# Optimization experiments

Hardware: AMD Instinct MI355X
Metric: run time of the kernel (lower is better)

Reference implementation:

```python
import jax, jax.numpy as jnp
import numpy as np

EMBED = 1024
HEADS = 16
HEAD_SIZE = EMBED // HEADS


def setup_inputs() -> dict:
    key = jax.random.key(0)
    ks = jax.random.split(key, 12)
    B, S = 2, 2048
    s = 1.0 / np.sqrt(EMBED)
    return {
        "querys": jax.random.normal(ks[0], (B, S, EMBED), jnp.float32),
        "keys": jax.random.normal(ks[1], (B, S, EMBED), jnp.float32),
        "values": jax.random.normal(ks[2], (B, S, EMBED), jnp.float32),
        "Wq": jax.random.normal(ks[3], (EMBED, EMBED), jnp.float32) * s,
        "bq": jax.random.normal(ks[4], (EMBED,), jnp.float32) * s,
        "Wk": jax.random.normal(ks[5], (EMBED, EMBED), jnp.float32) * s,
        "bk": jax.random.normal(ks[6], (EMBED,), jnp.float32) * s,
        "Wv": jax.random.normal(ks[7], (EMBED, EMBED), jnp.float32) * s,
        "bv": jax.random.normal(ks[8], (EMBED,), jnp.float32) * s,
        "Wo": jax.random.normal(ks[9], (EMBED, EMBED), jnp.float32) * s,
        "bo": jax.random.normal(ks[10], (EMBED,), jnp.float32) * s,
    }


def reference(querys, keys, values, Wq, bq, Wk, bk, Wv, bv, Wo, bo):
    B, S, E = querys.shape
    H, D = HEADS, HEAD_SIZE
    # torch nn.Linear: y = x @ W.T + b
    q = (querys @ Wq.T + bq).reshape(B, S, H, D).transpose(0, 2, 1, 3)  # [B,H,S,D]
    k = (keys @ Wk.T + bk).reshape(B, S, H, D).transpose(0, 2, 1, 3)
    v = (values @ Wv.T + bv).reshape(B, S, H, D).transpose(0, 2, 1, 3)
    # NOTE: original scales by head_size**0.05 (faithful to source, likely a bug)
    scale = D ** 0.05
    energy = jnp.einsum("bhqd,bhkd->bhqk", q, k) / scale  # [B,H,S,S]
    attention = jax.nn.softmax(energy, axis=-1)
    out = jnp.einsum("bhqk,bhkd->bhqd", attention, v)  # [B,H,S,D]
    out = out.transpose(0, 2, 1, 3).reshape(B, S, E)
    return out @ Wo.T + bo
```

## Files before the change

kernel.cpp:

```cpp
#include <hip/hip_runtime.h>

typedef __attribute__((ext_vector_type(4))) float f32x4;
typedef __attribute__((ext_vector_type(8))) float f32x8;
typedef __attribute__((ext_vector_type(8))) unsigned short ushort8;
typedef __attribute__((ext_vector_type(4))) unsigned short ushort4v;
typedef __attribute__((ext_vector_type(8))) __bf16 bf16x8;

#define QSCALE 1.17183256f

#if __has_builtin(__builtin_amdgcn_exp2f)
#define EXP2(x) __builtin_amdgcn_exp2f(x)
#else
#define EXP2(x) exp2f(x)
#endif

__device__ __forceinline__ unsigned short f2bf(float x) {
  unsigned u = __float_as_uint(x);
  u += 0x7FFFu + ((u >> 16) & 1u);
  return (unsigned short)(u >> 16);
}

__device__ __forceinline__ ushort8 cvt8(const float* src) {
  float4 x0 = *(const float4*)src;
  float4 x1 = *(const float4*)(src + 4);
  ushort8 v;
  v[0] = f2bf(x0.x); v[1] = f2bf(x0.y); v[2] = f2bf(x0.z); v[3] = f2bf(x0.w);
  v[4] = f2bf(x1.x); v[5] = f2bf(x1.y); v[6] = f2bf(x1.z); v[7] = f2bf(x1.w);
  return v;
}

__device__ __forceinline__ f32x4 mfma16(ushort8 a, ushort8 b, f32x4 c) {
  return __builtin_amdgcn_mfma_f32_16x16x32_bf16(
      __builtin_bit_cast(bf16x8, a), __builtin_bit_cast(bf16x8, b), c, 0, 0, 0);
}
__device__ __forceinline__ f32x4 mfma16b(bf16x8 a, ushort8 b, f32x4 c) {
  return __builtin_amdgcn_mfma_f32_16x16x32_bf16(
      a, __builtin_bit_cast(bf16x8, b), c, 0, 0, 0);
}

__device__ __forceinline__ void gload_lds16(const void* g, void* l) {
  __builtin_amdgcn_global_load_lds(
      (const __attribute__((address_space(1))) void*)g,
      (__attribute__((address_space(3))) void*)l, 16, 0, 0);
}

__global__ __launch_bounds__(256) void cvt_f32_bf16(
    const float* __restrict__ s0, const float* __restrict__ s1, const float* __restrict__ s2,
    const float* __restrict__ s3, const float* __restrict__ s4, const float* __restrict__ s5,
    const float* __restrict__ s6, unsigned short* __restrict__ dstA,
    unsigned short* __restrict__ dstW)
{
  const int z = blockIdx.y;
  const float* src;
  unsigned short* dst;
  int n;
  if (z < 3) {
    src = (z == 0) ? s0 : (z == 1) ? s1 : s2;
    dst = dstA + (size_t)z * 4194304;
    n = 4194304;
  } else {
    src = (z == 3) ? s3 : (z == 4) ? s4 : (z == 5) ? s5 : s6;
    dst = dstW + (size_t)(z - 3) * 1048576;
    n = 1048576;
  }
  int i = (blockIdx.x * 256 + threadIdx.x) * 8;
  const int stride = gridDim.x * 256 * 8;
  for (; i < n; i += stride) *(ushort8*)(dst + i) = cvt8(src + i);
}

__global__ __launch_bounds__(256) void gemm_qkv_bf(
    const unsigned short* __restrict__ Abf, const unsigned short* __restrict__ Wbf,
    const float* __restrict__ bq, const float* __restrict__ bk, const float* __restrict__ bv,
    unsigned short* __restrict__ Qb, unsigned short* __restrict__ Kb,
    unsigned short* __restrict__ Vtb)
{
  __shared__ __align__(16) unsigned short Sl[4][4096];
  const int lin = blockIdx.x + 8 * blockIdx.y + 256 * blockIdx.z;
  const int swz = (lin & 7) * 96 + (lin >> 3);
  const int bx = swz & 7, by = (swz >> 3) & 31, z = swz >> 8;

  const unsigned short* Ap = Abf + (size_t)z * 4194304;
  const unsigned short* Wp = Wbf + (size_t)z * 1048576;
  const float* bp = (z == 0) ? bq : (z == 1) ? bk : bv;

  const int t = threadIdx.x, l = t & 63, w = t >> 6;
  const int lr = l & 15, g = l >> 4;
  const int wm = (w >> 1) * 64, wn = (w & 1) * 64;

  int prow[2], pcol[2];
#pragma unroll
  for (int j = 0; j < 2; ++j) {
    int p = j * 256 + w * 64 + l;
    prow[j] = p >> 2;
    pcol[j] = (p & 3) ^ ((prow[j] >> 1) & 3);
  }

  char* lds0 = (char*)&Sl[0][0];
  const int arow0 = wm + lr, brow0 = wn + lr;
  const int abyte = (arow0 * 32 + (g ^ ((arow0 >> 1) & 3)) * 8) * 2;
  const int bbyte = 8192 + (brow0 * 32 + (g ^ ((brow0 >> 1) & 3)) * 8) * 2;

  f32x4 acc[4][4] = {};

#define STAGE_QKV(bufoff, k0)                                                     \
  {                                                                               \
    _Pragma("unroll") for (int j = 0; j < 2; ++j) {                               \
      gload_lds16(Ap + (size_t)(by * 128 + prow[j]) * 1024 + (k0) + pcol[j] * 8,  \
                  lds0 + (bufoff) + (j * 256 + w * 64) * 16);                     \
      gload_lds16(Wp + (size_t)(bx * 128 + prow[j]) * 1024 + (k0) + pcol[j] * 8,  \
                  lds0 + (bufoff) + 8192 + (j * 256 + w * 64) * 16);              \
    }                                                                             \
  }

  STAGE_QKV(0, 0)
  __syncthreads();

  for (int kt = 0; kt < 32; ++kt) {
    const int curoff = (kt & 1) << 14;
    if (kt < 31) STAGE_QKV(curoff ^ 16384, (kt + 1) * 32)
    const char* pa = lds0 + curoff;
    ushort8 a[4], b[4];
#pragma unroll
    for (int m = 0; m < 4; ++m)
      a[m] = *(const ushort8*)(pa + abyte + m * 1024);
#pragma unroll
    for (int n = 0; n < 4; ++n)
      b[n] = *(const ushort8*)(pa + bbyte + n * 1024);
#pragma unroll
    for (int m = 0; m < 4; ++m)
#pragma unroll
      for (int n = 0; n < 4; ++n)
        acc[m][n] = mfma16(a[m], b[n], acc[m][n]);
    __syncthreads();
  }

  float bias_n[4];
#pragma unroll
  for (int n = 0; n < 4; ++n) bias_n[n] = bp[bx * 128 + wn + n * 16 + lr];

  if (z < 2) {
    const float sc = (z == 0) ? QSCALE : 1.0f;
    unsigned short* Cp = z ? Kb : Qb;
#pragma unroll
    for (int m = 0; m < 4; ++m)
#pragma unroll
      for (int n = 0; n < 4; ++n)
#pragma unroll
        for (int r = 0; r < 4; ++r) {
          float v = (acc[m][n][r] + bias_n[n]) * sc;
          int gm = by * 128 + wm + m * 16 + g * 4 + r;
          int gn = bx * 128 + wn + n * 16 + lr;
          int bb = gm >> 11, s = gm & 2047;
          int h = gn >> 6, d = gn & 63;
          Cp[((size_t)((bb * 16 + h) * 2048 + s) << 6) + d] = f2bf(v);
        }
  } else {
#pragma unroll
    for (int m = 0; m < 4; ++m) {
      int gm0 = by * 128 + wm + m * 16 + g * 4;
      int bb = gm0 >> 11, s0 = gm0 & 2047;
#pragma unroll
      for (int n = 0; n < 4; ++n) {
        int gn = bx * 128 + wn + n * 16 + lr;
        int h = gn >> 6, d = gn & 63;
        ushort4v pk;
#pragma unroll
        for (int r = 0; r < 4; ++r) pk[r] = f2bf(acc[m][n][r] + bias_n[n]);
        *(ushort4v*)&Vtb[((size_t)((bb * 16 + h) * 64 + d) << 11) + s0] = pk;
      }
    }
  }
}

__global__ __launch_bounds__(256) void gemm_o_bf(
    const unsigned short* __restrict__ AO, const unsigned short* __restrict__ Wp,
    const float* __restrict__ bo, float* __restrict__ C)
{
  __shared__ __align__(16) unsigned short Al[2][128 * 32];
  __shared__ __align__(16) unsigned short Wl[2][64 * 32];
  const int lin = blockIdx.x + 16 * blockIdx.y;
  const int swz = (lin & 7) * 64 + (lin >> 3);
  const int bx = swz & 15, by = swz >> 4;

  const int t = threadIdx.x, l = t & 63, w = t >> 6;
  const int lr = l & 15, g = l >> 4;
  const int wm = w * 32;

  int prow[2], pcol[2];
#pragma unroll
  for (int j = 0; j < 2; ++j) {
    int p = j * 256 + w * 64 + l;
    prow[j] = p >> 2;
    pcol[j] = (p & 3) ^ ((prow[j] >> 1) & 3);
  }

  f32x4 acc[2][4] = {};

#define STAGE_O(buf, k0)                                                          \
  {                                                                               \
    _Pragma("unroll") for (int j = 0; j < 2; ++j) {                               \
      gload_lds16(AO + (size_t)(by * 128 + prow[j]) * 1024 + (k0) + pcol[j] * 8,  \
                  &Al[buf][(j * 256 + w * 64) * 8]);                              \
    }                                                                             \
    gload_lds16(Wp + (size_t)(bx * 64 + prow[0]) * 1024 + (k0) + pcol[0] * 8,     \
                &Wl[buf][(w * 64) * 8]);                                          \
  }

  STAGE_O(0, 0)
  __syncthreads();

  for (int kt = 0; kt < 32; ++kt) {
    const int cur = kt & 1;
    if (kt < 31) STAGE_O(cur ^ 1, (kt + 1) * 32)
    ushort8 a[2], b[4];
#pragma unroll
    for (int m = 0; m < 2; ++m) {
      int r = wm + m * 16 + lr;
      a[m] = *(const ushort8*)&Al[cur][r * 32 + (g ^ ((r >> 1) & 3)) * 8];
    }
#pragma unroll
    for (int n = 0; n < 4; ++n) {
      int r = n * 16 + lr;
      b[n] = *(const ushort8*)&Wl[cur][r * 32 + (g ^ ((r >> 1) & 3)) * 8];
    }
#pragma unroll
    for (int m = 0; m < 2; ++m)
#pragma unroll
      for (int n = 0; n < 4; ++n)
        acc[m][n] = mfma16(a[m], b[n], acc[m][n]);
    __syncthreads();
  }

  float bias_n[4];
#pragma unroll
  for (int n = 0; n < 4; ++n) bias_n[n] = bo[bx * 64 + n * 16 + lr];

#pragma unroll
  for (int m = 0; m < 2; ++m)
#pragma unroll
    for (int n = 0; n < 4; ++n)
#pragma unroll
      for (int r = 0; r < 4; ++r) {
        int gm = by * 128 + wm + m * 16 + g * 4 + r;
        int gn = bx * 64 + n * 16 + lr;
        C[(size_t)gm * 1024 + gn] = acc[m][n][r] + bias_n[n];
      }
}

__global__ __launch_bounds__(512) void attn_fwd(
    const unsigned short* __restrict__ Qb, const unsigned short* __restrict__ Kb,
    const unsigned short* __restrict__ Vtb, unsigned short* __restrict__ AO)
{
  __shared__ __align__(16) unsigned short Kl[4][64 * 64];
  __shared__ __align__(16) unsigned short Vl[4][64 * 64];
  const int t = threadIdx.x;
  const int l = t & 63, w = t >> 6;
  const int lr = l & 15, g = l >> 4;
  const int lin = blockIdx.x + 16 * blockIdx.y;
  const int swz = (lin & 7) * 64 + (lin >> 3);
  const int qt = swz & 15, bh = swz >> 4;

  const unsigned short* Qh = Qb + (size_t)bh * (2048 * 64);
  const unsigned short* Kh = Kb + (size_t)bh * (2048 * 64);
  const unsigned short* Vth = Vtb + (size_t)bh * (64 * 2048);

  ushort8 aq[2];
#pragma unroll
  for (int kk = 0; kk < 2; ++kk) {
    int q = qt * 128 + w * 16 + lr;
    aq[kk] = *(const ushort8*)&Qh[q * 64 + kk * 32 + g * 8];
  }

  ushort8 ones;
#pragma unroll
  for (int j = 0; j < 8; ++j) ones[j] = 0x3F80;

  f32x4 o[4] = {};
  f32x4 lacc = {};

  const int sr = t >> 3, sc = t & 7;
  ushort8 rk, rv;

#define STAGE_ATTN(buf)                                                      \
  {                                                                          \
    *(ushort8*)&Kl[buf][sr * 64 + ((sc ^ (sr & 7))) * 8] = rk;               \
    _Pragma("unroll") for (int h = 0; h < 2; ++h) {                          \
      int tw = 2 * sc + h;                                                   \
      int n4 = tw >> 2, gg = tw & 3;                                         \
      int chunk = ((n4 >> 1) << 2) + gg;                                     \
      int within = (n4 & 1) << 2;                                            \
      ushort4v hv = h ? __builtin_shufflevector(rv, rv, 4, 5, 6, 7)          \
                      : __builtin_shufflevector(rv, rv, 0, 1, 2, 3);         \
      *(ushort4v*)&Vl[buf][sr * 64 + ((chunk ^ (sr & 7))) * 8 + within] = hv;\
    }                                                                        \
  }

#define LOAD_NEXT(tile)                                                      \
  {                                                                          \
    rk = *(const ushort8*)&Kh[((tile) * 64 + sr) * 64 + sc * 8];             \
    rv = *(const ushort8*)&Vth[sr * 2048 + (tile) * 64 + sc * 8];            \
  }

#define COMPUTE_ATTN(cur)                                                    \
  {                                                                          \
    f32x4 s[4] = {};                                                         \
    __builtin_amdgcn_s_setprio(1);                                           \
    _Pragma("unroll") for (int kk = 0; kk < 2; ++kk) {                       \
      _Pragma("unroll") for (int n = 0; n < 4; ++n) {                        \
        ushort8 ak = *(const ushort8*)&Kl[cur][(n * 16 + lr) * 64 +          \
                                              (((kk * 4 + g) ^ (lr & 7))) * 8]; \
        s[n] = mfma16(ak, aq[kk], s[n]);                                     \
      }                                                                      \
    }                                                                        \
    __builtin_amdgcn_s_setprio(0);                                           \
    float p[4][4];                                                           \
    _Pragma("unroll") for (int n = 0; n < 4; ++n)                            \
      _Pragma("unroll") for (int r = 0; r < 4; ++r) p[n][r] = EXP2(s[n][r]); \
    f32x8 v0 = {p[0][0], p[0][1], p[0][2], p[0][3],                          \
                p[1][0], p[1][1], p[1][2], p[1][3]};                         \
    f32x8 v1 = {p[2][0], p[2][1], p[2][2], p[2][3],                          \
                p[3][0], p[3][1], p[3][2], p[3][3]};                         \
    bf16x8 pa[2];                                                            \
    pa[0] = __builtin_convertvector(v0, bf16x8);                             \
    pa[1] = __builtin_convertvector(v1, bf16x8);                             \
    __builtin_amdgcn_s_setprio(1);                                           \
    _Pragma("unroll") for (int kk = 0; kk < 2; ++kk) {                       \
      lacc = mfma16b(pa[kk], ones, lacc);                                    \
      _Pragma("unroll") for (int n = 0; n < 4; ++n) {                        \
        int d = n * 16 + lr;                                                 \
        ushort8 bv = *(const ushort8*)&Vl[cur][d * 64 +                      \
                                              (((kk * 4 + g) ^ (d & 7))) * 8]; \
        o[n] = mfma16b(pa[kk], bv, o[n]);                                    \
      }                                                                      \
    }                                                                        \
    __builtin_amdgcn_s_setprio(0);                                           \
  }

  LOAD_NEXT(0)
  STAGE_ATTN(0)
  LOAD_NEXT(1)
  STAGE_ATTN(1)
  __syncthreads();

  for (int jj = 0; jj < 8; ++jj) {
    LOAD_NEXT(4 * jj + 2)
    COMPUTE_ATTN(0)
    STAGE_ATTN(2)
    LOAD_NEXT(4 * jj + 3)
    COMPUTE_ATTN(1)
    STAGE_ATTN(3)
    __syncthreads();
    if (jj < 7) LOAD_NEXT(4 * jj + 4)
    COMPUTE_ATTN(2)
    if (jj < 7) STAGE_ATTN(0)
    if (jj < 7) LOAD_NEXT(4 * jj + 5)
    COMPUTE_ATTN(3)
    if (jj < 7) STAGE_ATTN(1)
    __syncthreads();
  }

  const int bb = bh >> 4, h = bh & 15;
  float inv[4];
#pragma unroll
  for (int r = 0; r < 4; ++r) inv[r] = 1.0f / lacc[r];
#pragma unroll
  for (int n = 0; n < 4; ++n)
#pragma unroll
    for (int r = 0; r < 4; ++r) {
      int q = qt * 128 + w * 16 + g * 4 + r;
      AO[(size_t)(bb * 2048 + q) * 1024 + h * 64 + n * 16 + lr] =
          f2bf(o[n][r] * inv[r]);
    }
}

__global__ __launch_bounds__(256) void gemm_qkv_f32(
    const float* __restrict__ Aq, const float* __restrict__ Ak, const float* __restrict__ Av,
    const float* __restrict__ Wq, const float* __restrict__ Wk, const float* __restrict__ Wv,
    const float* __restrict__ bq, const float* __restrict__ bk, const float* __restrict__ bv,
    unsigned short* __restrict__ Qb, unsigned short* __restrict__ Kb, unsigned short* __restrict__ Vtb)
{
  __shared__ __align__(16) unsigned short Al[128 * 32];
  __shared__ __align__(16) unsigned short Wl[128 * 32];
  const int z = blockIdx.z;
  const float* Ap = (z == 0) ? Aq : (z == 1) ? Ak : Av;
  const float* Wp = (z == 0) ? Wq : (z == 1) ? Wk : Wv;
  const float* bp = (z == 0) ? bq : (z == 1) ? bk : bv;

  const int t = threadIdx.x;
  const int l = t & 63, w = t >> 6;
  const int lr = l & 15, g = l >> 4;
  const int wm = (w >> 1) * 64, wn = (w & 1) * 64;
  const int bx = blockIdx.x, by = blockIdx.y;
  const int r0 = t >> 2, c0 = t & 3;

  f32x4 acc[4][4] = {};

  for (int k0 = 0; k0 < 1024; k0 += 32) {
    __syncthreads();
#pragma unroll
    for (int i = 0; i < 2; ++i) {
      int r = r0 + i * 64;
      int cs = c0 ^ ((r >> 1) & 3);
      *(ushort8*)&Al[r * 32 + cs * 8] = cvt8(Ap + (size_t)(by * 128 + r) * 1024 + k0 + c0 * 8);
      *(ushort8*)&Wl[r * 32 + cs * 8] = cvt8(Wp + (size_t)(bx * 128 + r) * 1024 + k0 + c0 * 8);
    }
    __syncthreads();
    ushort8 a[4], b[4];
#pragma unroll
    for (int m = 0; m < 4; ++m) {
      int r = wm + m * 16 + lr;
      a[m] = *(const ushort8*)&Al[r * 32 + (g ^ ((r >> 1) & 3)) * 8];
    }
#pragma unroll
    for (int n = 0; n < 4; ++n) {
      int r = wn + n * 16 + lr;
      b[n] = *(const ushort8*)&Wl[r * 32 + (g ^ ((r >> 1) & 3)) * 8];
    }
#pragma unroll
    for (int m = 0; m < 4; ++m)
#pragma unroll
      for (int n = 0; n < 4; ++n)
        acc[m][n] = mfma16(a[m], b[n], acc[m][n]);
  }

  float bias_n[4];
#pragma unroll
  for (int n = 0; n < 4; ++n) bias_n[n] = bp[bx * 128 + wn + n * 16 + lr];

  if (z < 2) {
    const float sc = (z == 0) ? QSCALE : 1.0f;
    unsigned short* Cp = z ? Kb : Qb;
#pragma unroll
    for (int m = 0; m < 4; ++m)
#pragma unroll
      for (int n = 0; n < 4; ++n)
#pragma unroll
        for (int r = 0; r < 4; ++r) {
          float v = (acc[m][n][r] + bias_n[n]) * sc;
          int gm = by * 128 + wm + m * 16 + g * 4 + r;
          int gn = bx * 128 + wn + n * 16 + lr;
          int bb = gm >> 11, s = gm & 2047;
          int h = gn >> 6, d = gn & 63;
          Cp[((size_t)((bb * 16 + h) * 2048 + s) << 6) + d] = f2bf(v);
        }
  } else {
#pragma unroll
    for (int m = 0; m < 4; ++m) {
      int gm0 = by * 128 + wm + m * 16 + g * 4;
      int bb = gm0 >> 11, s0 = gm0 & 2047;
#pragma unroll
      for (int n = 0; n < 4; ++n) {
        int gn = bx * 128 + wn + n * 16 + lr;
        int h = gn >> 6, d = gn & 63;
        ushort4v pk;
#pragma unroll
        for (int r = 0; r < 4; ++r) pk[r] = f2bf(acc[m][n][r] + bias_n[n]);
        *(ushort4v*)&Vtb[((size_t)((bb * 16 + h) * 64 + d) << 11) + s0] = pk;
      }
    }
  }
}

__global__ __launch_bounds__(256) void gemm_o_f32(
    const unsigned short* __restrict__ AO, const float* __restrict__ Wo,
    const float* __restrict__ bo, float* __restrict__ C)
{
  __shared__ __align__(16) unsigned short Al[128 * 32];
  __shared__ __align__(16) unsigned short Wl[64 * 32];
  const int t = threadIdx.x;
  const int l = t & 63, w = t >> 6;
  const int lr = l & 15, g = l >> 4;
  const int wm = w * 32;
  const int bx = blockIdx.x, by = blockIdx.y;
  const int r0 = t >> 2, c0 = t & 3;

  f32x4 acc[2][4] = {};

  for (int k0 = 0; k0 < 1024; k0 += 32) {
    __syncthreads();
#pragma unroll
    for (int i = 0; i < 2; ++i) {
      int r = r0 + i * 64;
      int cs = c0 ^ ((r >> 1) & 3);
      *(ushort8*)&Al[r * 32 + cs * 8] =
          *(const ushort8*)&AO[(size_t)(by * 128 + r) * 1024 + k0 + c0 * 8];
    }
    {
      int r = r0;
      int cs = c0 ^ ((r >> 1) & 3);
      *(ushort8*)&Wl[r * 32 + cs * 8] = cvt8(Wo + (size_t)(bx * 64 + r) * 1024 + k0 + c0 * 8);
    }
    __syncthreads();
    ushort8 a[2], b[4];
#pragma unroll
    for (int m = 0; m < 2; ++m) {
      int r = wm + m * 16 + lr;
      a[m] = *(const ushort8*)&Al[r * 32 + (g ^ ((r >> 1) & 3)) * 8];
    }
#pragma unroll
    for (int n = 0; n < 4; ++n) {
      int r = n * 16 + lr;
      b[n] = *(const ushort8*)&Wl[r * 32 + (g ^ ((r >> 1) & 3)) * 8];
    }
#pragma unroll
    for (int m = 0; m < 2; ++m)
#pragma unroll
      for (int n = 0; n < 4; ++n)
        acc[m][n] = mfma16(a[m], b[n], acc[m][n]);
  }

  float bias_n[4];
#pragma unroll
  for (int n = 0; n < 4; ++n) bias_n[n] = bo[bx * 64 + n * 16 + lr];

#pragma unroll
  for (int m = 0; m < 2; ++m)
#pragma unroll
    for (int n = 0; n < 4; ++n)
#pragma unroll
      for (int r = 0; r < 4; ++r) {
        int gm = by * 128 + wm + m * 16 + g * 4 + r;
        int gn = bx * 64 + n * 16 + lr;
        C[(size_t)gm * 1024 + gn] = acc[m][n][r] + bias_n[n];
      }
}

extern "C" void kernel_launch(void* const* d_in, const int* in_sizes, int n_in,
                              void* d_out, int out_size, void* d_ws, size_t ws_size,
                              hipStream_t stream) {
  (void)in_sizes; (void)n_in; (void)out_size;
  const float* querys = (const float*)d_in[0];
  const float* keys   = (const float*)d_in[1];
  const float* values = (const float*)d_in[2];
  const float* Wq = (const float*)d_in[3];
  const float* bq = (const float*)d_in[4];
  const float* Wk = (const float*)d_in[5];
  const float* bk = (const float*)d_in[6];
  const float* Wv = (const float*)d_in[7];
  const float* bv = (const float*)d_in[8];
  const float* Wo = (const float*)d_in[9];
  const float* bo = (const float*)d_in[10];

  const size_t need = (size_t)29360128 * 2;
  if (ws_size >= need) {
    unsigned short* Wbf = (unsigned short*)d_ws;
    unsigned short* Qb  = Wbf + 4194304;
    unsigned short* Kb  = Qb + 4194304;
    unsigned short* Vtb = Kb + 4194304;
    unsigned short* Abf = Vtb + 4194304;
    unsigned short* AO  = Abf;

    cvt_f32_bf16<<<dim3(1024, 7), 256, 0, stream>>>(querys, keys, values, Wq, Wk, Wv, Wo,
                                                    Abf, Wbf);
    gemm_qkv_bf<<<dim3(8, 32, 3), 256, 0, stream>>>(Abf, Wbf, bq, bk, bv, Qb, Kb, Vtb);
    attn_fwd<<<dim3(16, 32), 512, 0, stream>>>(Qb, Kb, Vtb, AO);
    gemm_o_bf<<<dim3(16, 32), 256, 0, stream>>>(AO, Wbf + 3 * 1048576, bo, (float*)d_out);
  } else {
    unsigned short* Qb  = (unsigned short*)d_ws;
    unsigned short* Kb  = Qb + (size_t)4194304;
    unsigned short* Vtb = Kb + (size_t)4194304;
    unsigned short* AO  = Vtb + (size_t)4194304;

    gemm_qkv_f32<<<dim3(8, 32, 3), 256, 0, stream>>>(querys, keys, values, Wq, Wk, Wv,
                                                     bq, bk, bv, Qb, Kb, Vtb);
    attn_fwd<<<dim3(16, 32), 512, 0, stream>>>(Qb, Kb, Vtb, AO);
    gemm_o_f32<<<dim3(16, 32), 256, 0, stream>>>(AO, Wo, bo, (float*)d_out);
  }
}
```

Before: 123.3 us.

## Split attention key tiles across warp pairs with 32-row query tiles per warp

Measured after the change: 120.4 us (median of 2 runs). 1.02x faster.

```diff
diff --git a/kernel.cpp b/kernel.cpp
--- a/kernel.cpp
+++ b/kernel.cpp
@@ -256,6 +256,7 @@
   const int t = threadIdx.x;
   const int l = t & 63, w = t >> 6;
   const int lr = l & 15, g = l >> 4;
+  const int wq = w & 3, kh = w >> 2;
   const int lin = blockIdx.x + 16 * blockIdx.y;
   const int swz = (lin & 7) * 64 + (lin >> 3);
   const int qt = swz & 15, bh = swz >> 4;
@@ -264,19 +265,21 @@
   const unsigned short* Kh = Kb + (size_t)bh * (2048 * 64);
   const unsigned short* Vth = Vtb + (size_t)bh * (64 * 2048);
 
-  ushort8 aq[2];
-#pragma unroll
-  for (int kk = 0; kk < 2; ++kk) {
-    int q = qt * 128 + w * 16 + lr;
-    aq[kk] = *(const ushort8*)&Qh[q * 64 + kk * 32 + g * 8];
-  }
+  ushort8 aq[2][2];
+#pragma unroll
+  for (int m = 0; m < 2; ++m)
+#pragma unroll
+    for (int kk = 0; kk < 2; ++kk) {
+      int q = qt * 128 + wq * 32 + m * 16 + lr;
+      aq[m][kk] = *(const ushort8*)&Qh[q * 64 + kk * 32 + g * 8];
+    }
 
   ushort8 ones;
 #pragma unroll
   for (int j = 0; j < 8; ++j) ones[j] = 0x3F80;
 
-  f32x4 o[4] = {};
-  f32x4 lacc = {};
+  f32x4 o[2][4] = {};
+  f32x4 lacc[2] = {};
 
   const int sr = t >> 3, sc = t & 7;
   ushort8 rk, rv;
@@ -303,35 +306,37 @@
 
 #define COMPUTE_ATTN(cur)                                                    \
   {                                                                          \
-    f32x4 s[4] = {};                                                         \
+    f32x4 s[2][2] = {};                                                      \
     __builtin_amdgcn_s_setprio(1);                                           \
     _Pragma("unroll") for (int kk = 0; kk < 2; ++kk) {                       \
-      _Pragma("unroll") for (int n = 0; n < 4; ++n) {                        \
-        ushort8 ak = *(const ushort8*)&Kl[cur][(n * 16 + lr) * 64 +          \
+      _Pragma("unroll") for (int n = 0; n < 2; ++n) {                        \
+        ushort8 ak = *(const ushort8*)&Kl[cur][(kh * 32 + n * 16 + lr) * 64 +\
                                               (((kk * 4 + g) ^ (lr & 7))) * 8]; \
-        s[n] = mfma16(ak, aq[kk], s[n]);                                     \
+        _Pragma("unroll") for (int m = 0; m < 2; ++m)                        \
+          s[n][m] = mfma16(ak, aq[m][kk], s[n][m]);                          \
       }                                                                      \
     }                                                                        \
     __builtin_amdgcn_s_setprio(0);                                           \
-    float p[4][4];                                                           \
-    _Pragma("unroll") for (int n = 0; n < 4; ++n)                            \
-      _Pragma("unroll") for (int r = 0; r < 4; ++r) p[n][r] = EXP2(s[n][r]); \
-    f32x8 v0 = {p[0][0], p[0][1], p[0][2], p[0][3],                          \
-                p[1][0], p[1][1], p[1][2], p[1][3]};                         \
-    f32x8 v1 = {p[2][0], p[2][1], p[2][2], p[2][3],                          \
-                p[3][0], p[3][1], p[3][2], p[3][3]};                         \
+    float p[2][2][4];                                                        \
+    _Pragma("unroll") for (int n = 0; n < 2; ++n)                            \
+      _Pragma("unroll") for (int m = 0; m < 2; ++m)                          \
+        _Pragma("unroll") for (int r = 0; r < 4; ++r)                        \
+          p[n][m][r] = EXP2(s[n][m][r]);                                     \
     bf16x8 pa[2];                                                            \
-    pa[0] = __builtin_convertvector(v0, bf16x8);                             \
-    pa[1] = __builtin_convertvector(v1, bf16x8);                             \
+    _Pragma("unroll") for (int m = 0; m < 2; ++m) {                          \
+      f32x8 v = {p[0][m][0], p[0][m][1], p[0][m][2], p[0][m][3],             \
+                 p[1][m][0], p[1][m][1], p[1][m][2], p[1][m][3]};            \
+      pa[m] = __builtin_convertvector(v, bf16x8);                            \
+    }                                                                        \
     __builtin_amdgcn_s_setprio(1);                                           \
-    _Pragma("unroll") for (int kk = 0; kk < 2; ++kk) {                       \
-      lacc = mfma16b(pa[kk], ones, lacc);                                    \
-      _Pragma("unroll") for (int n = 0; n < 4; ++n) {                        \
-        int d = n * 16 + lr;                                                 \
-        ushort8 bv = *(const ushort8*)&Vl[cur][d * 64 +                      \
-                                              (((kk * 4 + g) ^ (d & 7))) * 8]; \
-        o[n] = mfma16b(pa[kk], bv, o[n]);                                    \
-      }                                                                      \
+    _Pragma("unroll") for (int m = 0; m < 2; ++m)                            \
+      lacc[m] = mfma16b(pa[m], ones, lacc[m]);                               \
+    _Pragma("unroll") for (int n = 0; n < 4; ++n) {                          \
+      int d = n * 16 + lr;                                                   \
+      ushort8 bv = *(const ushort8*)&Vl[cur][d * 64 +                        \
+                                            (((kh * 4 + g) ^ (d & 7))) * 8]; \
+      _Pragma("unroll") for (int m = 0; m < 2; ++m)                          \
+        o[m][n] = mfma16b(pa[m], bv, o[m][n]);                               \
     }                                                                        \
     __builtin_amdgcn_s_setprio(0);                                           \
   }
@@ -359,18 +364,55 @@
     __syncthreads();
   }
 
-  const int bb = bh >> 4, h = bh & 15;
-  float inv[4];
-#pragma unroll
-  for (int r = 0; r < 4; ++r) inv[r] = 1.0f / lacc[r];
-#pragma unroll
-  for (int n = 0; n < 4; ++n)
-#pragma unroll
-    for (int r = 0; r < 4; ++r) {
-      int q = qt * 128 + w * 16 + g * 4 + r;
-      AO[(size_t)(bb * 2048 + q) * 1024 + h * 64 + n * 16 + lr] =
-          f2bf(o[n][r] * inv[r]);
-    }
+  __syncthreads();
+  float* Of = (float*)&Kl[0][0];
+  if (kh == 1) {
+#pragma unroll
+    for (int m = 0; m < 2; ++m)
+#pragma unroll
+      for (int n = 0; n < 4; ++n)
+#pragma unroll
+        for (int r = 0; r < 4; ++r)
+          Of[(wq * 32 + m * 16 + g * 4 + r) * 64 + n * 16 + lr] = o[m][n][r];
+  }
+  __syncthreads();
+  if (kh == 0) {
+#pragma unroll
+    for (int m = 0; m < 2; ++m)
+#pragma unroll
+      for (int n = 0; n < 4; ++n)
+#pragma unroll
+        for (int r = 0; r < 4; ++r)
+          o[m][n][r] += Of[(wq * 32 + m * 16 + g * 4 + r) * 64 + n * 16 + lr];
+  }
+  __syncthreads();
+  float* Lf = (float*)&Kl[0][0];
+  if (kh == 1 && lr == 0) {
+#pragma unroll
+    for (int m = 0; m < 2; ++m)
+#pragma unroll
+      for (int r = 0; r < 4; ++r)
+        Lf[wq * 32 + m * 16 + g * 4 + r] = lacc[m][r];
+  }
+  __syncthreads();
+  if (kh == 0) {
+    const int bb = bh >> 4, h = bh & 15;
+#pragma unroll
+    for (int m = 0; m < 2; ++m) {
+      float inv[4];
+#pragma unroll
+      for (int r = 0; r < 4; ++r)
+        inv[r] = 1.0f / (lacc[m][r] + Lf[wq * 32 + m * 16 + g * 4 + r]);
+#pragma unroll
+      for (int n = 0; n < 4; ++n)
+#pragma unroll
+        for (int r = 0; r < 4; ++r) {
+          int q = qt * 128 + wq * 32 + m * 16 + g * 4 + r;
+          AO[(size_t)(bb * 2048 + q) * 1024 + h * 64 + n * 16 + lr] =
+              f2bf(o[m][n][r] * inv[r]);
+        }
+    }
+  }
 }
 
 __global__ __launch_bounds__(256) void gemm_qkv_f32(
```
